# Kernel optimization log

Measured on AMD Instinct MI355X. Metric: run time of the kernel, lower is better.

Reference implementation:

```python
import jax, jax.numpy as jnp
import numpy as np

N, B, S, BW, IC = 512, 4, 31, 11, 32

def gelu(x):
    return jax.nn.gelu(x, approximate=False)

def conv2d(x, w, b, pad, groups=1):
    y = jax.lax.conv_general_dilated(x, w, (1, 1), [(pad, pad), (pad, pad)],
        dimension_numbers=('NCHW', 'OIHW', 'NCHW'), feature_group_count=groups)
    return y + b[None, :, None, None]

def extract_windows(fmap, pos, win):
    C, H, W = fmap.shape[1:]
    r = win // 2
    cx = jnp.round(pos[:, 0]).astype(jnp.int32)
    cy = jnp.round(pos[:, 1]).astype(jnp.int32)
    off = jnp.arange(win, dtype=jnp.int32) - r
    ys = jnp.clip(cy[:, None] + off[None, :], 0, H - 1)
    xs = jnp.clip(cx[:, None] + off[None, :], 0, W - 1)
    w = fmap[0][:, ys[:, :, None], xs[:, None, :]]
    return jnp.transpose(w, (1, 0, 2, 3))

def _forward(bottleneck, vis_stem, spv, ppb,
             ic1_w, ic1_b, ic2_w, ic2_b, ic3_w, ic3_b,
             cnx_dw_w, cnx_dw_b, cnx_ln_w, cnx_ln_b,
             cnx_pw1_w, cnx_pw1_b, cnx_pw2_w, cnx_pw2_b, cnx_gamma,
             bnp_w, bnp_b, band_embed, film_w, film_b,
             dec1_w, dec1_b, dec2_w, dec2_b, dec3_w, dec3_b,
             tile_h, tile_w, fused_h, fused_w, vis_h, vis_w):
    n = spv.shape[0]
    # intrinsic path: per-source stem window -> 3 convs
    sw = extract_windows(vis_stem, spv, S)                 # [N,64,S,S]
    h = gelu(conv2d(sw, ic1_w, ic1_b, 1))
    h = gelu(conv2d(h, ic2_w, ic2_b, 1))
    intrinsic = conv2d(h, ic3_w, ic3_b, 1)                 # [N,IC,S,S]
    # bottleneck context path (vis px -> fused px: scale by vis_scale/fused_scale)
    scale = 0.1 / 0.4
    pbn = spv * scale
    pbn = jnp.stack([jnp.clip(pbn[:, 0], 0.0, fused_w - 1.0),
                     jnp.clip(pbn[:, 1], 0.0, fused_h - 1.0)], axis=-1)
    bwin = extract_windows(bottleneck, pbn, BW)            # [N,256,BW,BW]
    d = conv2d(bwin, cnx_dw_w, cnx_dw_b, 3, groups=bwin.shape[1])
    d = jnp.transpose(d, (0, 2, 3, 1))                     # NHWC
    mu = d.mean(-1, keepdims=True)
    var = ((d - mu) ** 2).mean(-1, keepdims=True)
    d = (d - mu) / jnp.sqrt(var + 1e-6) * cnx_ln_w + cnx_ln_b
    d = gelu(d @ cnx_pw1_w.T + cnx_pw1_b)
    d = (d @ cnx_pw2_w.T + cnx_pw2_b) * cnx_gamma
    bwin = bwin + jnp.transpose(d, (0, 3, 1, 2))
    bn_feat = gelu(conv2d(bwin, bnp_w, bnp_b, 0))          # [N,64,BW,BW]
    # fixed gaussian-weighted pooling (sigma=0.4 on [-1,1] grid)
    lin = jnp.linspace(-1.0, 1.0, BW)
    yy, xx = jnp.meshgrid(lin, lin, indexing='ij')
    g = jnp.exp(-(xx ** 2 + yy ** 2) / (2 * 0.4 ** 2))
    g = g / g.sum()
    bn_vec = (bn_feat * g[None, None]).sum((-2, -1))       # [N,64]
    # FiLM conditioning
    tile_pos = jnp.clip(jnp.stack([ppb[..., 0] / max(tile_w - 1.0, 1.0),
                                   ppb[..., 1] / max(tile_h - 1.0, 1.0)], -1), 0.0, 1.0)
    sub_px = ppb - jnp.round(ppb)
    band_e = jnp.broadcast_to(band_embed[None], (n, B, band_embed.shape[1]))
    bn_nb = jnp.broadcast_to(bn_vec[:, None], (n, B, bn_vec.shape[1]))
    cond = jnp.concatenate([band_e, tile_pos, sub_px, bn_nb], axis=-1)  # [N,B,84]
    film = cond @ film_w.T + film_b                        # [N,B,2*IC]
    gamma = 1.0 + film[..., :IC]
    beta = film[..., IC:]
    mod = intrinsic[:, None] * gamma[..., None, None] + beta[..., None, None]
    mod = gelu(mod).reshape(n * B, IC, S, S)
    o = gelu(conv2d(mod, dec1_w, dec1_b, 1))
    o = gelu(conv2d(o, dec2_w, dec2_b, 1))
    o = conv2d(o, dec3_w, dec3_b, 0).reshape(n, B, S, S)
    o = jax.nn.softplus(o)
    sums = jnp.maximum(o.sum((-2, -1), keepdims=True), 1e-8)
    return o / sums

def setup_inputs():
    key = jax.random.key(0)
    ks = jax.random.split(key, 24)
    FH = FW = 256; VH = VW = 1024; TH = TW = 1024
    f32 = jnp.float32
    nrm = lambda k, shp, s=0.05: jax.random.normal(k, shp, dtype=f32) * s
    return {
        'bottleneck': nrm(ks[0], (1, 256, FH, FW), 1.0),
        'vis_stem': nrm(ks[1], (1, 64, VH, VW), 1.0),
        'source_positions_vis': jax.random.uniform(ks[2], (N, 2), dtype=f32, minval=0.0, maxval=VW - 1.0),
        'positions_per_band': jax.random.uniform(ks[3], (N, B, 2), dtype=f32, minval=0.0, maxval=TW - 1.0),
        'ic1_w': nrm(ks[4], (64, 64, 3, 3)), 'ic1_b': jnp.zeros((64,), f32),
        'ic2_w': nrm(ks[5], (64, 64, 3, 3)), 'ic2_b': jnp.zeros((64,), f32),
        'ic3_w': nrm(ks[6], (IC, 64, 3, 3)), 'ic3_b': jnp.zeros((IC,), f32),
        'cnx_dw_w': nrm(ks[7], (256, 1, 7, 7)), 'cnx_dw_b': jnp.zeros((256,), f32),
        'cnx_ln_w': jnp.ones((256,), f32), 'cnx_ln_b': jnp.zeros((256,), f32),
        'cnx_pw1_w': nrm(ks[8], (1024, 256)), 'cnx_pw1_b': jnp.zeros((1024,), f32),
        'cnx_pw2_w': nrm(ks[9], (256, 1024)), 'cnx_pw2_b': jnp.zeros((256,), f32),
        'cnx_gamma': jnp.full((256,), 0.1, f32),
        'bnp_w': nrm(ks[10], (64, 256, 1, 1)), 'bnp_b': jnp.zeros((64,), f32),
        'band_embed': nrm(ks[11], (B, 16), 1.0),
        'film_w': nrm(ks[12], (2 * IC, 84)), 'film_b': jnp.zeros((2 * IC,), f32),
        'dec1_w': nrm(ks[13], (32, IC, 3, 3)), 'dec1_b': jnp.zeros((32,), f32),
        'dec2_w': nrm(ks[14], (32, 32, 3, 3)), 'dec2_b': jnp.zeros((32,), f32),
        'dec3_w': nrm(ks[15], (1, 32, 1, 1)), 'dec3_b': jnp.zeros((1,), f32),
        'tile_h': TH, 'tile_w': TW, 'fused_h': FH, 'fused_w': FW, 'vis_h': VH, 'vis_w': VW,
    }

def reference(bottleneck, vis_stem, source_positions_vis, positions_per_band, ic1_w, ic1_b, ic2_w, ic2_b, ic3_w, ic3_b, cnx_dw_w, cnx_dw_b, cnx_ln_w, cnx_ln_b, cnx_pw1_w, cnx_pw1_b, cnx_pw2_w, cnx_pw2_b, cnx_gamma, bnp_w, bnp_b, band_embed, film_w, film_b, dec1_w, dec1_b, dec2_w, dec2_b, dec3_w, dec3_b, tile_h, tile_w, fused_h, fused_w, vis_h, vis_w):
    return _forward(bottleneck, vis_stem, source_positions_vis, positions_per_band, ic1_w, ic1_b, ic2_w, ic2_b, ic3_w, ic3_b, cnx_dw_w, cnx_dw_b, cnx_ln_w, cnx_ln_b, cnx_pw1_w, cnx_pw1_b, cnx_pw2_w, cnx_pw2_b, cnx_gamma, bnp_w, bnp_b, band_embed, film_w, film_b, dec1_w, dec1_b, dec2_w, dec2_b, dec3_w, dec3_b, tile_h, tile_w, fused_h, fused_w, vis_h, vis_w)
```

## Files before the change

kernel.cpp:

```cpp
#include <hip/hip_runtime.h>
#include <hip/hip_bf16.h>
#include <cstdint>
#include <cstddef>
#include <cmath>

#define DEV __device__ __forceinline__

typedef __attribute__((ext_vector_type(8))) short bf16x8;
typedef __attribute__((ext_vector_type(4))) float f32x4;

DEV float erf_fast(float x){
  float ax = fabsf(x);
  float t = __builtin_amdgcn_rcpf(fmaf(0.3275911f, ax, 1.f));
  float p = t*fmaf(t, fmaf(t, fmaf(t, fmaf(t, 1.061405429f, -1.453152027f),
             1.421413741f), -0.284496736f), 0.254829592f);
  float e = __expf(-ax*ax);
  float r = fmaf(-p, e, 1.f);
  return x >= 0.f ? r : -r;
}
DEV float gelu_f(float x){ return 0.5f*x*(1.0f + erf_fast(x*0.7071067811865476f)); }
DEV float softplus_f(float x){ return fmaxf(x,0.f) + log1pf(expf(-fabsf(x))); }
DEV unsigned short f2bf(float x){
  __hip_bfloat16 h = __float2bfloat16(x);
  return reinterpret_cast<unsigned short&>(h);
// ... 9 lines not shown
  int ntn[8], ntk[8], K[8], conv[8], base[8];
};

__global__ __launch_bounds__(256) void packall_k(PackJobs J)
{
  int blk = blockIdx.x;
  int j = 0;
#pragma unroll
  for (int i=1;i<8;++i) if (blk >= J.base[i]) j = i;
  int tid = (blk - J.base[j])*256 + threadIdx.x;
  const int ntk = J.ntk[j], K = J.K[j];
  int total = J.ntn[j]*ntk*64;
  if (tid >= total) return;
  int lane = tid & 63;
  int f = tid >> 6;
  int kt = f % ntk, nt = f / ntk;
  int row = nt*16 + (lane & 15);
  int k0 = kt*32 + (lane >> 4)*8;
  const float* src = J.src[j];
  unsigned short h[8];
  if (J.conv[j]) {
    const int Cin = K;
#pragma unroll
    for (int q=0;q<8;++q) {
      int k = k0 + q;
      int s = k / Cin;
      int ic = k - s*Cin;
      h[q] = f2bf(src[((size_t)row*Cin + ic)*9 + s]);
    }
  } else {
#pragma unroll
    for (int q=0;q<8;++q) h[q] = f2bf(src[(size_t)row*K + k0 + q]);
  }
  uint4 pk;
  pk.x = (unsigned)h[0] | ((unsigned)h[1]<<16);
  pk.y = (unsigned)h[2] | ((unsigned)h[3]<<16);
  pk.z = (unsigned)h[4] | ((unsigned)h[5]<<16);
  pk.w = (unsigned)h[6] | ((unsigned)h[7]<<16);
  *reinterpret_cast<uint4*>(J.dst[j] + (size_t)tid*8) = pk;
}

__global__ __launch_bounds__(256) void dwt_k(const float* __restrict__ w,
                                             float* __restrict__ wT)
{
  int k = blockIdx.x;
  int ch = threadIdx.x;
  wT[k*256 + ch] = w[(size_t)ch*49 + k];
}

__global__ __launch_bounds__(256) void extvwin_k(const float* __restrict__ vis,
                                                 const float* __restrict__ spv,
                                                 unsigned short* __restrict__ vwin)
{
  int il = blockIdx.x;
  int p = blockIdx.y*256 + threadIdx.x;
  if (p >= 1089) return;
  int wy = p/33, wx = p%33;
  unsigned short* dst = vwin + ((size_t)il*1089 + p)*64;
  if (wy==0 || wy==32 || wx==0 || wx==32) {
    uint4 z = {0,0,0,0};
#pragma unroll
    for (int q=0;q<8;++q) *reinterpret_cast<uint4*>(dst + q*8) = z;
    return;
  }
  int cx = (int)rintf(spv[il*2+0]);
  int cy = (int)rintf(spv[il*2+1]);
  int gy = min(max(cy + wy - 16, 0), 1023);
  int gx = min(max(cx + wx - 16, 0), 1023);
  const float* sp = vis + (size_t)gy*1024 + gx;
  unsigned short h[64];
#pragma unroll
  for (int c=0;c<64;++c) h[c] = f2bf(sp[(size_t)c<<20]);
#pragma unroll
  for (int q=0;q<8;++q) {
    uint4 pk;
    pk.x = (unsigned)h[q*8+0] | ((unsigned)h[q*8+1]<<16);
    pk.y = (unsigned)h[q*8+2] | ((unsigned)h[q*8+3]<<16);
    pk.z = (unsigned)h[q*8+4] | ((unsigned)h[q*8+5]<<16);
    pk.w = (unsigned)h[q*8+6] | ((unsigned)h[q*8+7]<<16);
    *reinterpret_cast<uint4*>(dst + q*8) = pk;
  }
}

__global__ __launch_bounds__(512,2) void convchain_k(
    const unsigned short* __restrict__ vwin,
    const unsigned short* __restrict__ Wp1, const float* __restrict__ B1,
    const unsigned short* __restrict__ Wp2, const float* __restrict__ B2,
    const unsigned short* __restrict__ Wp3, const float* __restrict__ B3,
    unsigned short* __restrict__ outI)
{
  const int item = blockIdx.x;
  const int y0 = blockIdx.y*8;
  const int t = threadIdx.x;
  const int w = t>>6, l = t&63, g = l>>4, l15 = l&15;

  __shared__ __align__(16) unsigned short bufIn[462*64];
  __shared__ __align__(16) unsigned short bufC1[396*64];
  unsigned short* bufC2 = bufIn;

  const uint4 z4 = {0,0,0,0};

  for (int u=t; u<396*8; u+=512)
    *reinterpret_cast<uint4*>(bufC1 + u*8) = z4;
  for (int u=t; u<462*8; u+=512) {
    int slot = u & 7;
    int rowi = u >> 3;
    int r = rowi/33;
    int wy = y0 - 2 + r;
    uint4 val = z4;
    if ((unsigned)wy < 33u)
      val = *reinterpret_cast<const uint4*>(
          vwin + ((size_t)item*1089 + wy*33 + (rowi - r*33))*64 + slot*8);
    int ds = slot ^ (rowi & 7);
    *reinterpret_cast<uint4*>(&bufIn[rowi*64 + ds*8]) = val;
  }
  __syncthreads();

  {
    int pbase[3], rowB[3]; bool pv[3];
#pragma unroll
    for (int pt=0; pt<3; ++pt) {
      int pd = (w*3+pt)*16 + l15;
      int pc = min(pd, 371);
      int ry = pc/31, rx = pc - ry*31;
      pbase[pt] = ry*33 + rx;
      rowB[pt] = ry*33 + rx + 1;
      int yab = y0 - 2 + ry;
      pv[pt] = (pd < 372) && ((unsigned)yab < 31u);
    }
    f32x4 a1[4][3];
#pragma unroll
    for (int o=0;o<4;++o)
#pragma unroll
      for (int pt=0;pt<3;++pt) a1[o][pt] = (f32x4){0.f,0.f,0.f,0.f};

    for (int kt=0; kt<18; ++kt) {
      int k0 = kt*32 + g*8;
      int s = k0 >> 6;
      int icg = (k0 - (s<<6)) >> 3;
      int roff = (s/3)*33 + (s - (s/3)*3);
      bf16x8 bf[3];
#pragma unroll
      for (int pt=0; pt<3; ++pt) {
        int rowi = pbase[pt] + roff;
        int ds = icg ^ (rowi & 7);
        bf[pt] = *reinterpret_cast<const bf16x8*>(&bufIn[rowi*64 + ds*8]);
      }
#pragma unroll
      for (int o=0; o<4; ++o) {
        bf16x8 af = *reinterpret_cast<const bf16x8*>(Wp1 + ((size_t)(o*18+kt)*64 + l)*8);
#pragma unroll
        for (int pt=0; pt<3; ++pt)
          a1[o][pt] = __builtin_amdgcn_mfma_f32_16x16x32_bf16(af, bf[pt], a1[o][pt], 0,0,0);
      }
    }
#pragma unroll
    for (int o=0; o<4; ++o) {
      float4 bv4 = *reinterpret_cast<const float4*>(B1 + o*16 + g*4);
      int sl = o*2 + (g>>1);
#pragma unroll
      for (int pt=0; pt<3; ++pt) {
        if (!pv[pt]) continue;
        float v0 = gelu_f(a1[o][pt][0] + bv4.x);
        float v1 = gelu_f(a1[o][pt][1] + bv4.y);
        float v2 = gelu_f(a1[o][pt][2] + bv4.z);
        float v3 = gelu_f(a1[o][pt][3] + bv4.w);
        uint2 pk;
        pk.x = (unsigned)f2bf(v0) | ((unsigned)f2bf(v1)<<16);
        pk.y = (unsigned)f2bf(v2) | ((unsigned)f2bf(v3)<<16);
        int phys = sl ^ (rowB[pt] & 7);
        *reinterpret_cast<uint2*>(&bufC1[rowB[pt]*64 + phys*8 + (g&1)*4]) = pk;
      }
    }
  }
  __syncthreads();

  for (int u=t; u<330*8; u+=512)
    *reinterpret_cast<uint4*>(bufC2 + u*8) = z4;
  __syncthreads();

  {
    int pbase[3], rowB[3]; bool pv[3];
#pragma unroll
    for (int pt=0; pt<3; ++pt) {
      int pd = (w*3+pt)*16 + l15;
      int pc = min(pd, 309);
      int ry = pc/31, rx = pc - ry*31;
      pbase[pt] = ry*33 + rx;
      rowB[pt] = ry*33 + rx + 1;
      int yab = y0 - 1 + ry;
      pv[pt] = (pd < 310) && ((unsigned)yab < 31u);
    }
    f32x4 a2[4][3];
#pragma unroll
    for (int o=0;o<4;++o)
#pragma unroll
      for (int pt=0;pt<3;++pt) a2[o][pt] = (f32x4){0.f,0.f,0.f,0.f};

    for (int kt=0; kt<18; ++kt) {
      int k0 = kt*32 + g*8;
      int s = k0 >> 6;
      int icg = (k0 - (s<<6)) >> 3;
      int roff = (s/3)*33 + (s - (s/3)*3);
      bf16x8 bf[3];
#pragma unroll
      for (int pt=0; pt<3; ++pt) {
        int rowi = pbase[pt] + roff;
        int ds = icg ^ (rowi & 7);
        bf[pt] = *reinterpret_cast<const bf16x8*>(&bufC1[rowi*64 + ds*8]);
      }
#pragma unroll
      for (int o=0; o<4; ++o) {
        bf16x8 af = *reinterpret_cast<const bf16x8*>(Wp2 + ((size_t)(o*18+kt)*64 + l)*8);
#pragma unroll
        for (int pt=0; pt<3; ++pt)
          a2[o][pt] = __builtin_amdgcn_mfma_f32_16x16x32_bf16(af, bf[pt], a2[o][pt], 0,0,0);
      }
    }
#pragma unroll
    for (int o=0; o<4; ++o) {
      float4 bv4 = *reinterpret_cast<const float4*>(B2 + o*16 + g*4);
      int sl = o*2 + (g>>1);
#pragma unroll
      for (int pt=0; pt<3; ++pt) {
        if (!pv[pt]) continue;
        float v0 = gelu_f(a2[o][pt][0] + bv4.x);
        float v1 = gelu_f(a2[o][pt][1] + bv4.y);
        float v2 = gelu_f(a2[o][pt][2] + bv4.z);
        float v3 = gelu_f(a2[o][pt][3] + bv4.w);
        uint2 pk;
        pk.x = (unsigned)f2bf(v0) | ((unsigned)f2bf(v1)<<16);
        pk.y = (unsigned)f2bf(v2) | ((unsigned)f2bf(v3)<<16);
        int phys = sl ^ (rowB[pt] & 7);
        *reinterpret_cast<uint2*>(&bufC2[rowB[pt]*64 + phys*8 + (g&1)*4]) = pk;
      }
    }
  }
  __syncthreads();

  {
    int pbase[2], gpos[2]; bool pv[2];
#pragma unroll
    for (int pt=0; pt<2; ++pt) {
      int pd = (w*2+pt)*16 + l15;
      int pc = min(pd, 247);
      int ry = pc/31, rx = pc - ry*31;
      pbase[pt] = ry*33 + rx;
      gpos[pt] = y0*31 + pd;
      pv[pt] = (pd < 248) && (gpos[pt] < 961);
    }
    f32x4 a3[2][2];
#pragma unroll
    for (int o=0;o<2;++o)
#pragma unroll
      for (int pt=0;pt<2;++pt) a3[o][pt] = (f32x4){0.f,0.f,0.f,0.f};

    for (int kt=0; kt<18; ++kt) {
      int k0 = kt*32 + g*8;
      int s = k0 >> 6;
      int icg = (k0 - (s<<6)) >> 3;
      int roff = (s/3)*33 + (s - (s/3)*3);
      bf16x8 bf[2];
#pragma unroll
      for (int pt=0; pt<2; ++pt) {
        int rowi = pbase[pt] + roff;
        int ds = icg ^ (rowi & 7);
        bf[pt] = *reinterpret_cast<const bf16x8*>(&bufC2[rowi*64 + ds*8]);
      }
#pragma unroll
      for (int o=0; o<2; ++o) {
        bf16x8 af = *reinterpret_cast<const bf16x8*>(Wp3 + ((size_t)(o*18+kt)*64 + l)*8);
#pragma unroll
        for (int pt=0; pt<2; ++pt)
          a3[o][pt] = __builtin_amdgcn_mfma_f32_16x16x32_bf16(af, bf[pt], a3[o][pt], 0,0,0);
      }
    }
#pragma unroll
    for (int o=0; o<2; ++o) {
      float4 bv4 = *reinterpret_cast<const float4*>(B3 + o*16 + g*4);
#pragma unroll
      for (int pt=0; pt<2; ++pt) {
        if (!pv[pt]) continue;
        float v0 = a3[o][pt][0] + bv4.x;
        float v1 = a3[o][pt][1] + bv4.y;
        float v2 = a3[o][pt][2] + bv4.z;
        float v3 = a3[o][pt][3] + bv4.w;
        uint2 pk;
        pk.x = (unsigned)f2bf(v0) | ((unsigned)f2bf(v1)<<16);
        pk.y = (unsigned)f2bf(v2) | ((unsigned)f2bf(v3)<<16);
        *reinterpret_cast<uint2*>(outI + ((size_t)item*961 + gpos[pt])*32 + o*16 + g*4) = pk;
      }
    }
  }
}

__global__ __launch_bounds__(512,4) void decfused3_k(
    const unsigned short* __restrict__ intc,
    const unsigned short* __restrict__ Wp1, const float* __restrict__ B1,
    const unsigned short* __restrict__ Wp2, const float* __restrict__ B2,
    const float* __restrict__ film,
    const float* __restrict__ w3, const float* __restrict__ b3,
    float* __restrict__ outf, float* __restrict__ sums)
{
  const int item = blockIdx.x;
  const int y0 = blockIdx.y*16;
  const int t = threadIdx.x;
  const int w = t>>6, l = t&63, g = l>>4, l15 = l&15;

  constexpr int PA = 660;
  constexpr int PB = 594;
  __shared__ __align__(16) unsigned short ldsA[4*PA*8];
  __shared__ __align__(16) unsigned short ldsB[4*PB*8];

  const int sit = item >> 2;
  const float* frow = film + (size_t)item*64;

  for (int u=t; u<4*PB; u+=512)
    *reinterpret_cast<uint4*>(ldsB + u*8) = (uint4){0,0,0,0};

  for (int u=t; u<PA*4; u+=512) {
    int slot = u & 3;
    int rowi = u >> 2;
    int r = rowi/33, col = rowi - r*33;
    int y = y0 + r - 2, x = col - 1;
    uint4 val = {0,0,0,0};
    if ((unsigned)y < 31u && (unsigned)x < 31u) {
      val = *reinterpret_cast<const uint4*>(intc + ((size_t)sit*961 + y*31 + x)*32 + slot*8);
      int c0 = slot*8;
      float4 g0 = *reinterpret_cast<const float4*>(frow + c0);
      float4 g1 = *reinterpret_cast<const float4*>(frow + c0 + 4);
      float4 b0 = *reinterpret_cast<const float4*>(frow + 32 + c0);
      float4 b1 = *reinterpret_cast<const float4*>(frow + 32 + c0 + 4);
      unsigned short x8[8] = {
        (unsigned short)(val.x&0xffff),(unsigned short)(val.x>>16),
        (unsigned short)(val.y&0xffff),(unsigned short)(val.y>>16),
        (unsigned short)(val.z&0xffff),(unsigned short)(val.z>>16),
        (unsigned short)(val.w&0xffff),(unsigned short)(val.w>>16)};
      unsigned short o8[8];
      o8[0]=f2bf(gelu_f(fmaf(bf2f(x8[0]), 1.f+g0.x, b0.x)));
      o8[1]=f2bf(gelu_f(fmaf(bf2f(x8[1]), 1.f+g0.y, b0.y)));
      o8[2]=f2bf(gelu_f(fmaf(bf2f(x8[2]), 1.f+g0.z, b0.z)));
      o8[3]=f2bf(gelu_f(fmaf(bf2f(x8[3]), 1.f+g0.w, b0.w)));
      o8[4]=f2bf(gelu_f(fmaf(bf2f(x8[4]), 1.f+g1.x, b1.x)));
      o8[5]=f2bf(gelu_f(fmaf(bf2f(x8[5]), 1.f+g1.y, b1.y)));
      o8[6]=f2bf(gelu_f(fmaf(bf2f(x8[6]), 1.f+g1.z, b1.z)));
      o8[7]=f2bf(gelu_f(fmaf(bf2f(x8[7]), 1.f+g1.w, b1.w)));
      val.x = (unsigned)o8[0] | ((unsigned)o8[1]<<16);
      val.y = (unsigned)o8[2] | ((unsigned)o8[3]<<16);
      val.z = (unsigned)o8[4] | ((unsigned)o8[5]<<16);
      val.w = (unsigned)o8[6] | ((unsigned)o8[7]<<16);
    }
    *reinterpret_cast<uint4*>(&ldsA[((size_t)slot*PA + rowi)*8]) = val;
  }
  __syncthreads();

  {
    int pbase[5], rowB[5]; bool pv[5];
#pragma unroll
    for (int pt=0; pt<5; ++pt) {
      int pd = (w*5+pt)*16 + l15;
      int pc = min(pd, 557);
      int ry = pc/31, rx = pc - ry*31;
      pbase[pt] = ry*33 + rx;
      rowB[pt] = ry*33 + rx + 1;
      int gy = y0 - 1 + ry;
      pv[pt] = (pd < 558) && ((unsigned)gy < 31u);
    }
    f32x4 a1[2][5];
#pragma unroll
    for (int o=0;o<2;++o)
#pragma unroll
      for (int pt=0;pt<5;++pt) a1[o][pt] = (f32x4){0.f,0.f,0.f,0.f};

    for (int kt=0; kt<9; ++kt) {
      int roff = (kt/3)*33 + (kt - (kt/3)*3);
      bf16x8 bf[5];
#pragma unroll
      for (int pt=0; pt<5; ++pt) {
        int rowi = pbase[pt] + roff;
        bf[pt] = *reinterpret_cast<const bf16x8*>(&ldsA[((size_t)g*PA + rowi)*8]);
      }
#pragma unroll
      for (int o=0; o<2; ++o) {
        bf16x8 af = *reinterpret_cast<const bf16x8*>(Wp1 + ((size_t)(o*9+kt)*64 + l)*8);
#pragma unroll
        for (int pt=0; pt<5; ++pt)
          a1[o][pt] = __builtin_amdgcn_mfma_f32_16x16x32_bf16(af, bf[pt], a1[o][pt], 0,0,0);
      }
    }
#pragma unroll
    for (int o=0; o<2; ++o) {
      float4 bv4 = *reinterpret_cast<const float4*>(B1 + o*16 + g*4);
      int sl = o*2 + (g>>1);
#pragma unroll
      for (int pt=0; pt<5; ++pt) {
        if (!pv[pt]) continue;
        float v0 = gelu_f(a1[o][pt][0] + bv4.x);
        float v1 = gelu_f(a1[o][pt][1] + bv4.y);
        float v2 = gelu_f(a1[o][pt][2] + bv4.z);
        float v3 = gelu_f(a1[o][pt][3] + bv4.w);
        uint2 pk;
        pk.x = (unsigned)f2bf(v0) | ((unsigned)f2bf(v1)<<16);
        pk.y = (unsigned)f2bf(v2) | ((unsigned)f2bf(v3)<<16);
        *reinterpret_cast<uint2*>(&ldsB[((size_t)sl*PB + rowB[pt])*8 + (g&1)*4]) = pk;
      }
    }
  }
  __syncthreads();

  float bsum = 0.f;
  {
    int pbase[4], gpos[4]; bool pv[4];
#pragma unroll
    for (int pt=0; pt<4; ++pt) {
      int pd = (w*4+pt)*16 + l15;
      int pc = min(pd, 495);
      int py = pc/31, px = pc - py*31;
      pbase[pt] = py*33 + px;
      gpos[pt] = y0*31 + pd;
      pv[pt] = (pd < 496) && (gpos[pt] < 961);
    }
    f32x4 a2[2][4];
#pragma unroll
    for (int o=0;o<2;++o)
#pragma unroll
      for (int pt=0;pt<4;++pt) a2[o][pt] = (f32x4){0.f,0.f,0.f,0.f};

    for (int kt=0; kt<9; ++kt) {
      int roff = (kt/3)*33 + (kt - (kt/3)*3);
      bf16x8 bf[4];
#pragma unroll
      for (int pt=0; pt<4; ++pt) {
        int rowi = pbase[pt] + roff;
        bf[pt] = *reinterpret_cast<const bf16x8*>(&ldsB[((size_t)g*PB + rowi)*8]);
      }
#pragma unroll
      for (int o=0; o<2; ++o) {
        bf16x8 af = *reinterpret_cast<const bf16x8*>(Wp2 + ((size_t)(o*9+kt)*64 + l)*8);
#pragma unroll
        for (int pt=0; pt<4; ++pt)
          a2[o][pt] = __builtin_amdgcn_mfma_f32_16x16x32_bf16(af, bf[pt], a2[o][pt], 0,0,0);
      }
    }

    float w3r[8];
#pragma unroll
    for (int o=0;o<2;++o) {
      float4 wv = *reinterpret_cast<const float4*>(w3 + o*16 + g*4);
      w3r[o*4+0]=wv.x; w3r[o*4+1]=wv.y; w3r[o*4+2]=wv.z; w3r[o*4+3]=wv.w;
    }
    float b3v = b3[0];
#pragma unroll
    for (int pt=0; pt<4; ++pt) {
      float part = 0.f;
#pragma unroll
      for (int o=0; o<2; ++o) {
        float4 bv4 = *reinterpret_cast<const float4*>(B2 + o*16 + g*4);
        float v0 = gelu_f(a2[o][pt][0] + bv4.x);
        float v1 = gelu_f(a2[o][pt][1] + bv4.y);
        float v2 = gelu_f(a2[o][pt][2] + bv4.z);
        float v3 = gelu_f(a2[o][pt][3] + bv4.w);
        part += v0*w3r[o*4+0] + v1*w3r[o*4+1] + v2*w3r[o*4+2] + v3*w3r[o*4+3];
      }
      part += __shfl_xor(part, 16);
      part += __shfl_xor(part, 32);
      float sp = softplus_f(part + b3v);
      if (pv[pt] && g==0) {
        outf[(size_t)item*961 + gpos[pt]] = sp;
        bsum += sp;
      }
    }
  }
  {
    float* redf = reinterpret_cast<float*>(ldsA);
    redf[t] = bsum;
    __syncthreads();
    for (int off=256; off>0; off>>=1) {
      if (t < off) redf[t] += redf[t+off];
      __syncthreads();
    }
    if (t==0) atomicAdd(&sums[item], redf[0]);
  }
}

__global__ __launch_bounds__(256,4) void dwfused4_k(
    const float* __restrict__ bott, const float* __restrict__ spv,
    const float* __restrict__ wT, const float* __restrict__ b,
    unsigned short* __restrict__ bwinT, unsigned short* __restrict__ dwout)
{
  const int n = blockIdx.x, cs = blockIdx.y*64, t = threadIdx.x;
  __shared__ float tile[121*66];

  float pxf = fminf(fmaxf(spv[n*2+0]*0.25f, 0.f), 255.f);
  float pyf = fminf(fmaxf(spv[n*2+1]*0.25f, 0.f), 255.f);
  int cx = (int)rintf(pxf), cy = (int)rintf(pyf);

  for (int idx=t; idx<121*32; idx+=256) {
    int j = idx/121, p = idx - j*121;
    int y = p/11, x = p - y*11;
    int gy = min(max(cy + y - 5, 0), 255);
    int gx = min(max(cx + x - 5, 0), 255);
    const float* s0 = bott + ((size_t)(cs+2*j)<<16) + (gy<<8) + gx;
    *reinterpret_cast<float2*>(&tile[p*66 + 2*j]) = (float2){s0[0], s0[65536]};
  }
  __syncthreads();

  for (int idx=t; idx<121*64; idx+=256) {
    int p = idx >> 6, c = idx & 63;
    bwinT[((size_t)n*121 + p)*256 + cs + c] = f2bf(tile[p*66 + c]);
  }

  const int c = t & 63, ph = t >> 6;
  const int ch = cs + c;
  const float bias = b[ch];

  for (int y=ph; y<11; y+=4) {
    float acc[11];
#pragma unroll
    for (int x=0;x<11;++x) acc[x] = bias;
#pragma unroll
    for (int dy=0; dy<7; ++dy) {
      int yy = y + dy - 3;
      if ((unsigned)yy < 11u) {
        float r[11];
#pragma unroll
        for (int k=0;k<11;++k) r[k] = tile[(yy*11+k)*66 + c];
        float w7[7];
#pragma unroll
        for (int j=0;j<7;++j) w7[j] = wT[(dy*7+j)*256 + ch];
#pragma unroll
        for (int x=0;x<11;++x) {
#pragma unroll
          for (int dx=0;dx<7;++dx) {
            int xx = x + dx - 3;
            if (xx >= 0 && xx < 11)
              acc[x] = fmaf(r[xx], w7[dx], acc[x]);
          }
        }
      }
    }
#pragma unroll
    for (int x=0;x<11;++x)
      dwout[((size_t)n*121 + y*11 + x)*256 + ch] = f2bf(acc[x]);
  }
}

__global__ __launch_bounds__(512,4) void cnx_mfma3_k(
    const unsigned short* __restrict__ xin,
    const float* __restrict__ lnw, const float* __restrict__ lnb,
    const unsigned short* __restrict__ W1p, const float* __restrict__ B1,
    const unsigned short* __restrict__ W2p, const float* __restrict__ B2,
    const float* __restrict__ gvec,
    const unsigned short* __restrict__ bwinT,
    const unsigned short* __restrict__ Wbp, const float* __restrict__ bnpb,
    float* __restrict__ bnv, float inv_gsum)
{
  const int t = threadIdx.x;
  const int w = t >> 6;
  const int l = t & 63;
  const int g = l >> 4;
  const int l15 = l & 15;
  const int row0 = blockIdx.x * 64;

  __shared__ __align__(16) unsigned short xs[64*264];
  __shared__ __align__(16) unsigned short hs[64*136];
// ... 166 lines not shown
  }
}

__global__ __launch_bounds__(256) void film_k(
    const float* __restrict__ bn_vec, const float* __restrict__ ppb,
    const float* __restrict__ bemb, const float* __restrict__ fw,
    const float* __restrict__ fb, float* __restrict__ film)
{
  int n = blockIdx.x, t = threadIdx.x;
  __shared__ float cond[4][84];
  for (int i=t; i<4*84; i+=256) {
    int b = i/84, j = i%84;
    float v;
    if (j < 16) v = bemb[b*16 + j];
    else if (j == 16) { float p = ppb[((size_t)n*4+b)*2+0]; v = fminf(fmaxf(p*(1.f/1023.f),0.f),1.f); }
    else if (j == 17) { float p = ppb[((size_t)n*4+b)*2+1]; v = fminf(fmaxf(p*(1.f/1023.f),0.f),1.f); }
    else if (j == 18) { float p = ppb[((size_t)n*4+b)*2+0]; v = p - rintf(p); }
    else if (j == 19) { float p = ppb[((size_t)n*4+b)*2+1]; v = p - rintf(p); }
    else v = bn_vec[n*64 + (j-20)];
    cond[b][j] = v;
  }
  __syncthreads();
  int b = t >> 6, oc = t & 63;
  float s = fb[oc];
  for (int j=0;j<84;++j) s = fmaf(cond[b][j], fw[oc*84+j], s);
  film[((size_t)n*4+b)*64 + oc] = s;
}

__global__ __launch_bounds__(256) void norm_k(float* __restrict__ out,
                                              const float* __restrict__ sums)
{
  int il = blockIdx.x;
  int p = blockIdx.y*256 + threadIdx.x;
  if (p < 961) {
    float inv = 1.f / fmaxf(sums[il], 1e-8f);
    out[(size_t)il*961 + p] *= inv;
  }
}

extern "C" void kernel_launch(void* const* d_in, const int* in_sizes, int n_in,
                              void* d_out, int out_size, void* d_ws, size_t ws_size,
                              hipStream_t stream)
{
  const float* bott = (const float*)d_in[0];
  const float* vis  = (const float*)d_in[1];
  const float* spv  = (const float*)d_in[2];
  const float* ppb  = (const float*)d_in[3];
  const float* ic1w = (const float*)d_in[4];  const float* ic1b = (const float*)d_in[5];
  const float* ic2w = (const float*)d_in[6];  const float* ic2b = (const float*)d_in[7];
  const float* ic3w = (const float*)d_in[8];  const float* ic3b = (const float*)d_in[9];
  const float* dww  = (const float*)d_in[10]; const float* dwb  = (const float*)d_in[11];
  const float* lnw  = (const float*)d_in[12]; const float* lnb  = (const float*)d_in[13];
  const float* pw1w = (const float*)d_in[14]; const float* pw1b = (const float*)d_in[15];
  const float* pw2w = (const float*)d_in[16]; const float* pw2b = (const float*)d_in[17];
  const float* cgam = (const float*)d_in[18];
  const float* bnpw = (const float*)d_in[19]; const float* bnpb = (const float*)d_in[20];
  const float* bemb = (const float*)d_in[21];
  const float* fw   = (const float*)d_in[22]; const float* fb   = (const float*)d_in[23];
  const float* d1w  = (const float*)d_in[24]; const float* d1b  = (const float*)d_in[25];
  const float* d2w  = (const float*)d_in[26]; const float* d2b  = (const float*)d_in[27];
  const float* d3w  = (const float*)d_in[28]; const float* d3b  = (const float*)d_in[29];
  float* out = (float*)d_out;

  char* ws = (char*)d_ws;

  unsigned short* bwinT = (unsigned short*)(ws);
  unsigned short* dwout = (unsigned short*)(ws + 31719424);
  unsigned short* vwin  = (unsigned short*)(ws);
  unsigned short* bufI  = (unsigned short*)(ws + 71368704);
  size_t tail = 102858752;

  float* bnv  = (float*)(ws + tail);
  float* sums = (float*)(ws + tail + 131072);
  float* film = (float*)(ws + tail + 139264);
  unsigned short* W1p = (unsigned short*)(ws + tail + 663552);
  unsigned short* W2p = (unsigned short*)(ws + tail + 1187840);
  unsigned short* Wbp = (unsigned short*)(ws + tail + 1712128);
  unsigned short* Pc1 = (unsigned short*)(ws + tail + 1744896);
  unsigned short* Pc2 = (unsigned short*)(ws + tail + 1818624);
  unsigned short* Pc3 = (unsigned short*)(ws + tail + 1892352);
  unsigned short* Pd1 = (unsigned short*)(ws + tail + 1929216);
  unsigned short* Pd2 = (unsigned short*)(ws + tail + 1947648);
  float* dwwT = (float*)(ws + tail + 1966080);

  {
    PackJobs J;
    const float* srcs[8] = {pw1w, pw2w, bnpw, ic1w, ic2w, ic3w, d1w, d2w};
    unsigned short* dsts[8] = {W1p, W2p, Wbp, Pc1, Pc2, Pc3, Pd1, Pd2};
    int ntns[8] = {64,16,4, 4,4,2, 2,2};
    int ntks[8] = {8,32,8, 18,18,18, 9,9};
    int Ks[8]   = {256,1024,256, 64,64,64, 32,32};
    int convs[8]= {0,0,0, 1,1,1, 1,1};
    int base = 0;
    for (int i=0;i<8;++i) {
      J.src[i]=srcs[i]; J.dst[i]=dsts[i]; J.ntn[i]=ntns[i]; J.ntk[i]=ntks[i];
      J.K[i]=Ks[i]; J.conv[i]=convs[i]; J.base[i]=base;
      base += (ntns[i]*ntks[i]*64 + 255)/256;
    }
    packall_k<<<base,256,0,stream>>>(J);
  }
  dwt_k<<<49,256,0,stream>>>(dww, dwwT);

  hipMemsetAsync(ws + tail, 0, 139264, stream);

  float gs = 0.f;
  for (int py=0; py<11; ++py) for (int px=0; px<11; ++px) {
    float ly=-1.f+0.2f*py, lx=-1.f+0.2f*px;
    gs += expf(-(lx*lx+ly*ly)/0.32f);
  }
  const float inv_gsum = 1.f/gs;

  dwfused4_k<<<dim3(512,4),256,0,stream>>>(bott, spv, dwwT, dwb, bwinT, dwout);
  cnx_mfma3_k<<<968,512,0,stream>>>(dwout, lnw,lnb, W1p,pw1b, W2p,pw2b, cgam,
                                    bwinT, Wbp, bnpb, bnv, inv_gsum);
  film_k<<<512,256,0,stream>>>(bnv, ppb, bemb, fw, fb, film);

  extvwin_k<<<dim3(512,5),256,0,stream>>>(vis, spv, vwin);
  convchain_k<<<dim3(512,4),512,0,stream>>>(vwin, Pc1,ic1b, Pc2,ic2b, Pc3,ic3b, bufI);
  decfused3_k<<<dim3(2048,2),512,0,stream>>>(bufI, Pd1,d1b, Pd2,d2b,
      film, d3w, d3b, out, sums);
  norm_k<<<dim3(2048,4),256,0,stream>>>(out, sums);
}
```

Before: 699.9 us.

## Shrink conv-chain row tiles, precompute FiLM-GELU activations, use wave-shuffle reduction

The intrinsic conv chain now processes 4 output rows per block instead of 8, with smaller LDS buffers and launch bounds raised to 4 blocks per CU, to improve occupancy at the cost of more halo recomputation. The FiLM modulation and GELU, previously recomputed for each decoder halo tile, move into a separate modgen kernel that writes a modulated bf16 buffer per item. This adds a 4x-expanded global read and write. The decoder's block-level LDS tree reduction is replaced by wave shuffles plus one atomic per wave.

```diff
diff --git a/kernel.cpp b/kernel.cpp
--- a/kernel.cpp
+++ b/kernel.cpp
@@ -115,7 +115,7 @@
   }
 }
 
-__global__ __launch_bounds__(512,2) void convchain_k(
+__global__ __launch_bounds__(512,4) void convchain4_k(
     const unsigned short* __restrict__ vwin,
     const unsigned short* __restrict__ Wp1, const float* __restrict__ B1,
     const unsigned short* __restrict__ Wp2, const float* __restrict__ B2,
@@ -123,19 +123,19 @@
     unsigned short* __restrict__ outI)
 {
   const int item = blockIdx.x;
-  const int y0 = blockIdx.y*8;
+  const int y0 = blockIdx.y*4;
   const int t = threadIdx.x;
   const int w = t>>6, l = t&63, g = l>>4, l15 = l&15;
 
-  __shared__ __align__(16) unsigned short bufIn[462*64];
-  __shared__ __align__(16) unsigned short bufC1[396*64];
+  __shared__ __align__(16) unsigned short bufIn[330*64];
+  __shared__ __align__(16) unsigned short bufC1[264*64];
   unsigned short* bufC2 = bufIn;
 
   const uint4 z4 = {0,0,0,0};
 
-  for (int u=t; u<396*8; u+=512)
+  for (int u=t; u<264*8; u+=512)
     *reinterpret_cast<uint4*>(bufC1 + u*8) = z4;
-  for (int u=t; u<462*8; u+=512) {
+  for (int u=t; u<330*8; u+=512) {
     int slot = u & 7;
     int rowi = u >> 3;
     int r = rowi/33;
@@ -150,31 +150,31 @@
   __syncthreads();
 
   {
-    int pbase[3], rowB[3]; bool pv[3];
-#pragma unroll
-    for (int pt=0; pt<3; ++pt) {
-      int pd = (w*3+pt)*16 + l15;
-      int pc = min(pd, 371);
+    int pbase[2], rowB[2]; bool pv[2];
+#pragma unroll
+    for (int pt=0; pt<2; ++pt) {
+      int pd = (w*2+pt)*16 + l15;
+      int pc = min(pd, 247);
       int ry = pc/31, rx = pc - ry*31;
       pbase[pt] = ry*33 + rx;
       rowB[pt] = ry*33 + rx + 1;
       int yab = y0 - 2 + ry;
-      pv[pt] = (pd < 372) && ((unsigned)yab < 31u);
-    }
-    f32x4 a1[4][3];
+      pv[pt] = (pd < 248) && ((unsigned)yab < 31u);
+    }
+    f32x4 a1[4][2];
 #pragma unroll
     for (int o=0;o<4;++o)
 #pragma unroll
-      for (int pt=0;pt<3;++pt) a1[o][pt] = (f32x4){0.f,0.f,0.f,0.f};
+      for (int pt=0;pt<2;++pt) a1[o][pt] = (f32x4){0.f,0.f,0.f,0.f};
 
     for (int kt=0; kt<18; ++kt) {
       int k0 = kt*32 + g*8;
       int s = k0 >> 6;
       int icg = (k0 - (s<<6)) >> 3;
       int roff = (s/3)*33 + (s - (s/3)*3);
-      bf16x8 bf[3];
-#pragma unroll
-      for (int pt=0; pt<3; ++pt) {
+      bf16x8 bf[2];
+#pragma unroll
+      for (int pt=0; pt<2; ++pt) {
         int rowi = pbase[pt] + roff;
         int ds = icg ^ (rowi & 7);
         bf[pt] = *reinterpret_cast<const bf16x8*>(&bufIn[rowi*64 + ds*8]);
@@ -183,7 +183,7 @@
       for (int o=0; o<4; ++o) {
         bf16x8 af = *reinterpret_cast<const bf16x8*>(Wp1 + ((size_t)(o*18+kt)*64 + l)*8);
 #pragma unroll
-        for (int pt=0; pt<3; ++pt)
+        for (int pt=0; pt<2; ++pt)
           a1[o][pt] = __builtin_amdgcn_mfma_f32_16x16x32_bf16(af, bf[pt], a1[o][pt], 0,0,0);
       }
     }
@@ -192,7 +192,7 @@
       float4 bv4 = *reinterpret_cast<const float4*>(B1 + o*16 + g*4);
       int sl = o*2 + (g>>1);
 #pragma unroll
-      for (int pt=0; pt<3; ++pt) {
+      for (int pt=0; pt<2; ++pt) {
         if (!pv[pt]) continue;
         float v0 = gelu_f(a1[o][pt][0] + bv4.x);
         float v1 = gelu_f(a1[o][pt][1] + bv4.y);
@@ -208,36 +208,36 @@
   }
   __syncthreads();
 
-  for (int u=t; u<330*8; u+=512)
+  for (int u=t; u<198*8; u+=512)
     *reinterpret_cast<uint4*>(bufC2 + u*8) = z4;
   __syncthreads();
 
   {
-    int pbase[3], rowB[3]; bool pv[3];
-#pragma unroll
-    for (int pt=0; pt<3; ++pt) {
-      int pd = (w*3+pt)*16 + l15;
-      int pc = min(pd, 309);
+    int pbase[2], rowB[2]; bool pv[2];
+#pragma unroll
+    for (int pt=0; pt<2; ++pt) {
+      int pd = (w*2+pt)*16 + l15;
+      int pc = min(pd, 185);
       int ry = pc/31, rx = pc - ry*31;
       pbase[pt] = ry*33 + rx;
       rowB[pt] = ry*33 + rx + 1;
       int yab = y0 - 1 + ry;
-      pv[pt] = (pd < 310) && ((unsigned)yab < 31u);
-    }
-    f32x4 a2[4][3];
+      pv[pt] = (pd < 186) && ((unsigned)yab < 31u);
+    }
+    f32x4 a2[4][2];
 #pragma unroll
     for (int o=0;o<4;++o)
 #pragma unroll
-      for (int pt=0;pt<3;++pt) a2[o][pt] = (f32x4){0.f,0.f,0.f,0.f};
+      for (int pt=0;pt<2;++pt) a2[o][pt] = (f32x4){0.f,0.f,0.f,0.f};
 
     for (int kt=0; kt<18; ++kt) {
       int k0 = kt*32 + g*8;
       int s = k0 >> 6;
       int icg = (k0 - (s<<6)) >> 3;
       int roff = (s/3)*33 + (s - (s/3)*3);
-      bf16x8 bf[3];
-#pragma unroll
-      for (int pt=0; pt<3; ++pt) {
+      bf16x8 bf[2];
+#pragma unroll
+      for (int pt=0; pt<2; ++pt) {
         int rowi = pbase[pt] + roff;
         int ds = icg ^ (rowi & 7);
         bf[pt] = *reinterpret_cast<const bf16x8*>(&bufC1[rowi*64 + ds*8]);
@@ -246,7 +246,7 @@
       for (int o=0; o<4; ++o) {
         bf16x8 af = *reinterpret_cast<const bf16x8*>(Wp2 + ((size_t)(o*18+kt)*64 + l)*8);
 #pragma unroll
-        for (int pt=0; pt<3; ++pt)
+        for (int pt=0; pt<2; ++pt)
           a2[o][pt] = __builtin_amdgcn_mfma_f32_16x16x32_bf16(af, bf[pt], a2[o][pt], 0,0,0);
       }
     }
@@ -255,7 +255,7 @@
       float4 bv4 = *reinterpret_cast<const float4*>(B2 + o*16 + g*4);
       int sl = o*2 + (g>>1);
 #pragma unroll
-      for (int pt=0; pt<3; ++pt) {
+      for (int pt=0; pt<2; ++pt) {
         if (!pv[pt]) continue;
         float v0 = gelu_f(a2[o][pt][0] + bv4.x);
         float v1 = gelu_f(a2[o][pt][1] + bv4.y);
@@ -272,66 +272,90 @@
   __syncthreads();
 
   {
-    int pbase[2], gpos[2]; bool pv[2];
-#pragma unroll
-    for (int pt=0; pt<2; ++pt) {
-      int pd = (w*2+pt)*16 + l15;
-      int pc = min(pd, 247);
-      int ry = pc/31, rx = pc - ry*31;
-      pbase[pt] = ry*33 + rx;
-      gpos[pt] = y0*31 + pd;
-      pv[pt] = (pd < 248) && (gpos[pt] < 961);
-    }
-    f32x4 a3[2][2];
-#pragma unroll
-    for (int o=0;o<2;++o)
-#pragma unroll
-      for (int pt=0;pt<2;++pt) a3[o][pt] = (f32x4){0.f,0.f,0.f,0.f};
+    int pd = w*16 + l15;
+    int pc = min(pd, 123);
+    int ry = pc/31, rx = pc - ry*31;
+    int pbase = ry*33 + rx;
+    int gpos = y0*31 + pd;
+    bool pv = (pd < 124) && (gpos < 961);
+
+    f32x4 a3[2];
+#pragma unroll
+    for (int o=0;o<2;++o) a3[o] = (f32x4){0.f,0.f,0.f,0.f};
 
     for (int kt=0; kt<18; ++kt) {
       int k0 = kt*32 + g*8;
       int s = k0 >> 6;
       int icg = (k0 - (s<<6)) >> 3;
       int roff = (s/3)*33 + (s - (s/3)*3);
-      bf16x8 bf[2];
-#pragma unroll
-      for (int pt=0; pt<2; ++pt) {
-        int rowi = pbase[pt] + roff;
-        int ds = icg ^ (rowi & 7);
-        bf[pt] = *reinterpret_cast<const bf16x8*>(&bufC2[rowi*64 + ds*8]);
-      }
+      int rowi = pbase + roff;
+      int ds = icg ^ (rowi & 7);
+      bf16x8 bf = *reinterpret_cast<const bf16x8*>(&bufC2[rowi*64 + ds*8]);
 #pragma unroll
       for (int o=0; o<2; ++o) {
         bf16x8 af = *reinterpret_cast<const bf16x8*>(Wp3 + ((size_t)(o*18+kt)*64 + l)*8);
-#pragma unroll
-        for (int pt=0; pt<2; ++pt)
-          a3[o][pt] = __builtin_amdgcn_mfma_f32_16x16x32_bf16(af, bf[pt], a3[o][pt], 0,0,0);
-      }
-    }
-#pragma unroll
-    for (int o=0; o<2; ++o) {
-      float4 bv4 = *reinterpret_cast<const float4*>(B3 + o*16 + g*4);
-#pragma unroll
-      for (int pt=0; pt<2; ++pt) {
-        if (!pv[pt]) continue;
-        float v0 = a3[o][pt][0] + bv4.x;
-        float v1 = a3[o][pt][1] + bv4.y;
-        float v2 = a3[o][pt][2] + bv4.z;
-        float v3 = a3[o][pt][3] + bv4.w;
+        a3[o] = __builtin_amdgcn_mfma_f32_16x16x32_bf16(af, bf, a3[o], 0,0,0);
+      }
+    }
+    if (pv) {
+#pragma unroll
+      for (int o=0; o<2; ++o) {
+        float4 bv4 = *reinterpret_cast<const float4*>(B3 + o*16 + g*4);
+        float v0 = a3[o][0] + bv4.x;
+        float v1 = a3[o][1] + bv4.y;
+        float v2 = a3[o][2] + bv4.z;
+        float v3 = a3[o][3] + bv4.w;
         uint2 pk;
         pk.x = (unsigned)f2bf(v0) | ((unsigned)f2bf(v1)<<16);
         pk.y = (unsigned)f2bf(v2) | ((unsigned)f2bf(v3)<<16);
-        *reinterpret_cast<uint2*>(outI + ((size_t)item*961 + gpos[pt])*32 + o*16 + g*4) = pk;
-      }
-    }
-  }
-}
-
-__global__ __launch_bounds__(512,4) void decfused3_k(
-    const unsigned short* __restrict__ intc,
+        *reinterpret_cast<uint2*>(outI + ((size_t)item*961 + gpos)*32 + o*16 + g*4) = pk;
+      }
+    }
+  }
+}
+
+__global__ __launch_bounds__(256) void modgen_k(
+    const unsigned short* __restrict__ intc, const float* __restrict__ film,
+    unsigned short* __restrict__ mod)
+{
+  int idx = blockIdx.x*256 + threadIdx.x;
+  int slot = idx & 3;
+  int rest = idx >> 2;
+  int pos = rest % 961;
+  int item = rest / 961;
+  int sit = item >> 2;
+  const float* fr = film + (size_t)item*64 + slot*8;
+  uint4 val = *reinterpret_cast<const uint4*>(intc + ((size_t)sit*961 + pos)*32 + slot*8);
+  float4 g0 = *reinterpret_cast<const float4*>(fr);
+  float4 g1 = *reinterpret_cast<const float4*>(fr + 4);
+  float4 b0 = *reinterpret_cast<const float4*>(fr + 32);
+  float4 b1 = *reinterpret_cast<const float4*>(fr + 36);
+  unsigned short x8[8] = {
+    (unsigned short)(val.x&0xffff),(unsigned short)(val.x>>16),
+    (unsigned short)(val.y&0xffff),(unsigned short)(val.y>>16),
+    (unsigned short)(val.z&0xffff),(unsigned short)(val.z>>16),
+    (unsigned short)(val.w&0xffff),(unsigned short)(val.w>>16)};
+  unsigned short o8[8];
+  o8[0]=f2bf(gelu_f(fmaf(bf2f(x8[0]), 1.f+g0.x, b0.x)));
+  o8[1]=f2bf(gelu_f(fmaf(bf2f(x8[1]), 1.f+g0.y, b0.y)));
+  o8[2]=f2bf(gelu_f(fmaf(bf2f(x8[2]), 1.f+g0.z, b0.z)));
+  o8[3]=f2bf(gelu_f(fmaf(bf2f(x8[3]), 1.f+g0.w, b0.w)));
+  o8[4]=f2bf(gelu_f(fmaf(bf2f(x8[4]), 1.f+g1.x, b1.x)));
+  o8[5]=f2bf(gelu_f(fmaf(bf2f(x8[5]), 1.f+g1.y, b1.y)));
+  o8[6]=f2bf(gelu_f(fmaf(bf2f(x8[6]), 1.f+g1.z, b1.z)));
+  o8[7]=f2bf(gelu_f(fmaf(bf2f(x8[7]), 1.f+g1.w, b1.w)));
+  uint4 pk;
+  pk.x = (unsigned)o8[0] | ((unsigned)o8[1]<<16);
+  pk.y = (unsigned)o8[2] | ((unsigned)o8[3]<<16);
+  pk.z = (unsigned)o8[4] | ((unsigned)o8[5]<<16);
+  pk.w = (unsigned)o8[6] | ((unsigned)o8[7]<<16);
+  *reinterpret_cast<uint4*>(mod + (size_t)idx*8) = pk;
+}
+
+__global__ __launch_bounds__(512,4) void decfused4_k(
+    const unsigned short* __restrict__ mod,
     const unsigned short* __restrict__ Wp1, const float* __restrict__ B1,
     const unsigned short* __restrict__ Wp2, const float* __restrict__ B2,
-    const float* __restrict__ film,
     const float* __restrict__ w3, const float* __restrict__ b3,
     float* __restrict__ outf, float* __restrict__ sums)
 {
@@ -344,9 +368,6 @@
   constexpr int PB = 594;
   __shared__ __align__(16) unsigned short ldsA[4*PA*8];
   __shared__ __align__(16) unsigned short ldsB[4*PB*8];
-
-  const int sit = item >> 2;
-  const float* frow = film + (size_t)item*64;
 
   for (int u=t; u<4*PB; u+=512)
     *reinterpret_cast<uint4*>(ldsB + u*8) = (uint4){0,0,0,0};
@@ -357,32 +378,8 @@
     int r = rowi/33, col = rowi - r*33;
     int y = y0 + r - 2, x = col - 1;
     uint4 val = {0,0,0,0};
-    if ((unsigned)y < 31u && (unsigned)x < 31u) {
-      val = *reinterpret_cast<const uint4*>(intc + ((size_t)sit*961 + y*31 + x)*32 + slot*8);
-      int c0 = slot*8;
-      float4 g0 = *reinterpret_cast<const float4*>(frow + c0);
-      float4 g1 = *reinterpret_cast<const float4*>(frow + c0 + 4);
-      float4 b0 = *reinterpret_cast<const float4*>(frow + 32 + c0);
-      float4 b1 = *reinterpret_cast<const float4*>(frow + 32 + c0 + 4);
-      unsigned short x8[8] = {
-        (unsigned short)(val.x&0xffff),(unsigned short)(val.x>>16),
-        (unsigned short)(val.y&0xffff),(unsigned short)(val.y>>16),
-        (unsigned short)(val.z&0xffff),(unsigned short)(val.z>>16),
-        (unsigned short)(val.w&0xffff),(unsigned short)(val.w>>16)};
-      unsigned short o8[8];
-      o8[0]=f2bf(gelu_f(fmaf(bf2f(x8[0]), 1.f+g0.x, b0.x)));
-      o8[1]=f2bf(gelu_f(fmaf(bf2f(x8[1]), 1.f+g0.y, b0.y)));
-      o8[2]=f2bf(gelu_f(fmaf(bf2f(x8[2]), 1.f+g0.z, b0.z)));
-      o8[3]=f2bf(gelu_f(fmaf(bf2f(x8[3]), 1.f+g0.w, b0.w)));
-      o8[4]=f2bf(gelu_f(fmaf(bf2f(x8[4]), 1.f+g1.x, b1.x)));
-      o8[5]=f2bf(gelu_f(fmaf(bf2f(x8[5]), 1.f+g1.y, b1.y)));
-      o8[6]=f2bf(gelu_f(fmaf(bf2f(x8[6]), 1.f+g1.z, b1.z)));
-      o8[7]=f2bf(gelu_f(fmaf(bf2f(x8[7]), 1.f+g1.w, b1.w)));
-      val.x = (unsigned)o8[0] | ((unsigned)o8[1]<<16);
-      val.y = (unsigned)o8[2] | ((unsigned)o8[3]<<16);
-      val.z = (unsigned)o8[4] | ((unsigned)o8[5]<<16);
-      val.w = (unsigned)o8[6] | ((unsigned)o8[7]<<16);
-    }
+    if ((unsigned)y < 31u && (unsigned)x < 31u)
+      val = *reinterpret_cast<const uint4*>(mod + ((size_t)item*961 + y*31 + x)*32 + slot*8);
     *reinterpret_cast<uint4*>(&ldsA[((size_t)slot*PA + rowi)*8]) = val;
   }
   __syncthreads();
@@ -504,16 +501,13 @@
       }
     }
   }
-  {
-    float* redf = reinterpret_cast<float*>(ldsA);
-    redf[t] = bsum;
-    __syncthreads();
-    for (int off=256; off>0; off>>=1) {
-      if (t < off) redf[t] += redf[t+off];
-      __syncthreads();
-    }
-    if (t==0) atomicAdd(&sums[item], redf[0]);
-  }
+  bsum += __shfl_xor(bsum, 1);
+  bsum += __shfl_xor(bsum, 2);
+  bsum += __shfl_xor(bsum, 4);
+  bsum += __shfl_xor(bsum, 8);
+  bsum += __shfl_xor(bsum, 16);
+  bsum += __shfl_xor(bsum, 32);
+  if (l == 0) atomicAdd(&sums[item], bsum);
 }
 
 __global__ __launch_bounds__(256,4) void dwfused4_k(
@@ -846,6 +840,7 @@
   unsigned short* Pd1 = (unsigned short*)(ws + tail + 1929216);
   unsigned short* Pd2 = (unsigned short*)(ws + tail + 1947648);
   float* dwwT = (float*)(ws + tail + 1966080);
+  unsigned short* modb = (unsigned short*)(ws + 112000000);
 
   {
     PackJobs J;
@@ -880,8 +875,9 @@
   film_k<<<512,256,0,stream>>>(bnv, ppb, bemb, fw, fb, film);
 
   extvwin_k<<<dim3(512,5),256,0,stream>>>(vis, spv, vwin);
-  convchain_k<<<dim3(512,4),512,0,stream>>>(vwin, Pc1,ic1b, Pc2,ic2b, Pc3,ic3b, bufI);
-  decfused3_k<<<dim3(2048,2),512,0,stream>>>(bufI, Pd1,d1b, Pd2,d2b,
-      film, d3w, d3b, out, sums);
+  convchain4_k<<<dim3(512,8),512,0,stream>>>(vwin, Pc1,ic1b, Pc2,ic2b, Pc3,ic3b, bufI);
+  modgen_k<<<30752,256,0,stream>>>(bufI, film, modb);
+  decfused4_k<<<dim3(2048,2),512,0,stream>>>(modb, Pd1,d1b, Pd2,d2b,
+      d3w, d3b, out, sums);
   norm_k<<<dim3(2048,4),256,0,stream>>>(out, sums);
 }
```

Measured after the change: 903.9 us. 29.1% more time.

## Split FiLM+GELU modulation into separate kernel and use wave-shuffle reduction

Applied to the files above, without the earlier changes.

Precomputes the FiLM-modulated GELU activations for every item in a standalone kernel and writes them to a workspace buffer. The decoder then only loads the modulated tile, so halo rows shared by the two y-blocks are no longer recomputed. The block-level shared-memory reduction of the softplus sums becomes wave shuffles with one atomic per wave. This adds a large intermediate write and reread through global memory plus an extra kernel launch.

```diff
diff --git a/kernel.cpp b/kernel.cpp
--- a/kernel.cpp
+++ b/kernel.cpp
@@ -327,11 +327,48 @@
   }
 }
 
-__global__ __launch_bounds__(512,4) void decfused3_k(
-    const unsigned short* __restrict__ intc,
+__global__ __launch_bounds__(256) void modgen_k(
+    const unsigned short* __restrict__ intc, const float* __restrict__ film,
+    unsigned short* __restrict__ mod)
+{
+  int idx = blockIdx.x*256 + threadIdx.x;
+  int slot = idx & 3;
+  int rest = idx >> 2;
+  int pos = rest % 961;
+  int item = rest / 961;
+  int sit = item >> 2;
+  const float* fr = film + (size_t)item*64 + slot*8;
+  uint4 val = *reinterpret_cast<const uint4*>(intc + ((size_t)sit*961 + pos)*32 + slot*8);
+  float4 g0 = *reinterpret_cast<const float4*>(fr);
+  float4 g1 = *reinterpret_cast<const float4*>(fr + 4);
+  float4 b0 = *reinterpret_cast<const float4*>(fr + 32);
+  float4 b1 = *reinterpret_cast<const float4*>(fr + 36);
+  unsigned short x8[8] = {
+    (unsigned short)(val.x&0xffff),(unsigned short)(val.x>>16),
+    (unsigned short)(val.y&0xffff),(unsigned short)(val.y>>16),
+    (unsigned short)(val.z&0xffff),(unsigned short)(val.z>>16),
+    (unsigned short)(val.w&0xffff),(unsigned short)(val.w>>16)};
+  unsigned short o8[8];
+  o8[0]=f2bf(gelu_f(fmaf(bf2f(x8[0]), 1.f+g0.x, b0.x)));
+  o8[1]=f2bf(gelu_f(fmaf(bf2f(x8[1]), 1.f+g0.y, b0.y)));
+  o8[2]=f2bf(gelu_f(fmaf(bf2f(x8[2]), 1.f+g0.z, b0.z)));
+  o8[3]=f2bf(gelu_f(fmaf(bf2f(x8[3]), 1.f+g0.w, b0.w)));
+  o8[4]=f2bf(gelu_f(fmaf(bf2f(x8[4]), 1.f+g1.x, b1.x)));
+  o8[5]=f2bf(gelu_f(fmaf(bf2f(x8[5]), 1.f+g1.y, b1.y)));
+  o8[6]=f2bf(gelu_f(fmaf(bf2f(x8[6]), 1.f+g1.z, b1.z)));
+  o8[7]=f2bf(gelu_f(fmaf(bf2f(x8[7]), 1.f+g1.w, b1.w)));
+  uint4 pk;
+  pk.x = (unsigned)o8[0] | ((unsigned)o8[1]<<16);
+  pk.y = (unsigned)o8[2] | ((unsigned)o8[3]<<16);
+  pk.z = (unsigned)o8[4] | ((unsigned)o8[5]<<16);
+  pk.w = (unsigned)o8[6] | ((unsigned)o8[7]<<16);
+  *reinterpret_cast<uint4*>(mod + (size_t)idx*8) = pk;
+}
+
+__global__ __launch_bounds__(512,4) void decfused4_k(
+    const unsigned short* __restrict__ mod,
     const unsigned short* __restrict__ Wp1, const float* __restrict__ B1,
     const unsigned short* __restrict__ Wp2, const float* __restrict__ B2,
-    const float* __restrict__ film,
     const float* __restrict__ w3, const float* __restrict__ b3,
     float* __restrict__ outf, float* __restrict__ sums)
 {
@@ -344,9 +381,6 @@
   constexpr int PB = 594;
   __shared__ __align__(16) unsigned short ldsA[4*PA*8];
   __shared__ __align__(16) unsigned short ldsB[4*PB*8];
-
-  const int sit = item >> 2;
-  const float* frow = film + (size_t)item*64;
 
   for (int u=t; u<4*PB; u+=512)
     *reinterpret_cast<uint4*>(ldsB + u*8) = (uint4){0,0,0,0};
@@ -357,32 +391,8 @@
     int r = rowi/33, col = rowi - r*33;
     int y = y0 + r - 2, x = col - 1;
     uint4 val = {0,0,0,0};
-    if ((unsigned)y < 31u && (unsigned)x < 31u) {
-      val = *reinterpret_cast<const uint4*>(intc + ((size_t)sit*961 + y*31 + x)*32 + slot*8);
-      int c0 = slot*8;
-      float4 g0 = *reinterpret_cast<const float4*>(frow + c0);
-      float4 g1 = *reinterpret_cast<const float4*>(frow + c0 + 4);
-      float4 b0 = *reinterpret_cast<const float4*>(frow + 32 + c0);
-      float4 b1 = *reinterpret_cast<const float4*>(frow + 32 + c0 + 4);
-      unsigned short x8[8] = {
-        (unsigned short)(val.x&0xffff),(unsigned short)(val.x>>16),
-        (unsigned short)(val.y&0xffff),(unsigned short)(val.y>>16),
-        (unsigned short)(val.z&0xffff),(unsigned short)(val.z>>16),
-        (unsigned short)(val.w&0xffff),(unsigned short)(val.w>>16)};
-      unsigned short o8[8];
-      o8[0]=f2bf(gelu_f(fmaf(bf2f(x8[0]), 1.f+g0.x, b0.x)));
-      o8[1]=f2bf(gelu_f(fmaf(bf2f(x8[1]), 1.f+g0.y, b0.y)));
-      o8[2]=f2bf(gelu_f(fmaf(bf2f(x8[2]), 1.f+g0.z, b0.z)));
-      o8[3]=f2bf(gelu_f(fmaf(bf2f(x8[3]), 1.f+g0.w, b0.w)));
-      o8[4]=f2bf(gelu_f(fmaf(bf2f(x8[4]), 1.f+g1.x, b1.x)));
-      o8[5]=f2bf(gelu_f(fmaf(bf2f(x8[5]), 1.f+g1.y, b1.y)));
-      o8[6]=f2bf(gelu_f(fmaf(bf2f(x8[6]), 1.f+g1.z, b1.z)));
-      o8[7]=f2bf(gelu_f(fmaf(bf2f(x8[7]), 1.f+g1.w, b1.w)));
-      val.x = (unsigned)o8[0] | ((unsigned)o8[1]<<16);
-      val.y = (unsigned)o8[2] | ((unsigned)o8[3]<<16);
-      val.z = (unsigned)o8[4] | ((unsigned)o8[5]<<16);
-      val.w = (unsigned)o8[6] | ((unsigned)o8[7]<<16);
-    }
+    if ((unsigned)y < 31u && (unsigned)x < 31u)
+      val = *reinterpret_cast<const uint4*>(mod + ((size_t)item*961 + y*31 + x)*32 + slot*8);
     *reinterpret_cast<uint4*>(&ldsA[((size_t)slot*PA + rowi)*8]) = val;
   }
   __syncthreads();
@@ -504,16 +514,13 @@
       }
     }
   }
-  {
-    float* redf = reinterpret_cast<float*>(ldsA);
-    redf[t] = bsum;
-    __syncthreads();
-    for (int off=256; off>0; off>>=1) {
-      if (t < off) redf[t] += redf[t+off];
-      __syncthreads();
-    }
-    if (t==0) atomicAdd(&sums[item], redf[0]);
-  }
+  bsum += __shfl_xor(bsum, 1);
+  bsum += __shfl_xor(bsum, 2);
+  bsum += __shfl_xor(bsum, 4);
+  bsum += __shfl_xor(bsum, 8);
+  bsum += __shfl_xor(bsum, 16);
+  bsum += __shfl_xor(bsum, 32);
+  if (l == 0) atomicAdd(&sums[item], bsum);
 }
 
 __global__ __launch_bounds__(256,4) void dwfused4_k(
@@ -846,6 +853,7 @@
   unsigned short* Pd1 = (unsigned short*)(ws + tail + 1929216);
   unsigned short* Pd2 = (unsigned short*)(ws + tail + 1947648);
   float* dwwT = (float*)(ws + tail + 1966080);
+  unsigned short* modb = (unsigned short*)(ws + 112000000);
 
   {
     PackJobs J;
@@ -881,7 +889,8 @@
 
   extvwin_k<<<dim3(512,5),256,0,stream>>>(vis, spv, vwin);
   convchain_k<<<dim3(512,4),512,0,stream>>>(vwin, Pc1,ic1b, Pc2,ic2b, Pc3,ic3b, bufI);
-  decfused3_k<<<dim3(2048,2),512,0,stream>>>(bufI, Pd1,d1b, Pd2,d2b,
-      film, d3w, d3b, out, sums);
+  modgen_k<<<30752,256,0,stream>>>(bufI, film, modb);
+  decfused4_k<<<dim3(2048,2),512,0,stream>>>(modb, Pd1,d1b, Pd2,d2b,
+      d3w, d3b, out, sums);
   norm_k<<<dim3(2048,4),256,0,stream>>>(out, sums);
 }
```

Result: slower. 722.9 us (+3.3%).
